# Optimization experiments

Hardware: AMD Instinct MI355X
Metric: run time of the kernel (lower is better)

Reference implementation:

```python
import jax, jax.numpy as jnp
import numpy as np

B, T, TA = 16, 512, 1024
D_REG, D_AUD, HID, HEADS = 512, 512, 256, 4
NREG = 4  # mouth, left_eye, right_eye, nose (dict order)
N = NREG * B * T + B * TA  # total graph nodes


def _build_edges():
    # Faithful, vectorized version of build_graph's edge construction (phoneme_times=None).
    bs = np.arange(B)[:, None]
    ts = np.arange(T)[None, :]
    src, dst = [], []
    # cross-region same-timestep edges, all ordered pairs i != j (edge_attr 0)
    for i in range(NREG):
        for j in range(NREG):
            if i != j:
                n1 = i * B * T + bs * T + ts
                n2 = j * B * T + bs * T + ts
                src.append(n1.ravel()); dst.append(n2.ravel())
    # temporal edges within each region (edge_attr 1)
    tt = np.arange(T - 1)[None, :]
    for i in range(NREG):
        n1 = i * B * T + bs * T + tt
        src.append(n1.ravel()); dst.append((n1 + 1).ravel())
    # eye (region idx 1,2) -> audio alignment edges (edge_attr 3)
    t_aud = (np.arange(T)[None, :] * TA) // T
    audio_start = NREG * B * T
    for i in (1, 2):
        n_eye = i * B * T + bs * T + ts
        n_aud = audio_start + bs * TA + t_aud
        src.append(n_eye.ravel()); dst.append(np.broadcast_to(n_aud, (B, T)).ravel())
    # self loops (PyG GATConv default add_self_loops=True)
    loops = np.arange(N)
    src.append(loops); dst.append(loops)
    return np.concatenate(src).astype(np.int32), np.concatenate(dst).astype(np.int32)


def setup_inputs() -> dict:
    key = jax.random.key(0)
    ks = iter(jax.random.split(key, 48))
    def rn(shape, scale=1.0):
        return jax.random.normal(next(ks), shape, dtype=jnp.float32) * jnp.float32(scale)
    src_np, dst_np = _build_edges()
    inp = {
        'mouth': rn((B, T, D_REG)), 'left_eye': rn((B, T, D_REG)),
        'right_eye': rn((B, T, D_REG)), 'nose': rn((B, T, D_REG)),
        'audio_embeddings': rn((B, TA, D_AUD)),
    }
    s = 1.0 / np.sqrt(D_REG)
    for name in ['mouth', 'left_eye', 'right_eye', 'nose']:
        inp['w_' + name] = rn((D_REG, HID), s)
        inp['b_' + name] = jnp.zeros((HID,), jnp.float32)
    inp['w_audio'] = rn((D_AUD, HID), 1.0 / np.sqrt(D_AUD))
    inp['b_audio'] = jnp.zeros((HID,), jnp.float32)
    # GAT layers: layer 0 in=HID, layers 1,2 in=HID*HEADS; layers 0,1 concat, layer 2 averages heads
    dims_in = [HID, HID * HEADS, HID * HEADS]
    for l, din in enumerate(dims_in):
        concat = l < 2
        inp[f'W{l}'] = rn((din, HEADS * HID), 1.0 / np.sqrt(din))
        inp[f'as{l}'] = rn((HEADS, HID), 0.1)
        inp[f'ad{l}'] = rn((HEADS, HID), 0.1)
        inp[f'bias{l}'] = jnp.zeros((HEADS * HID,) if concat else (HID,), jnp.float32)
    inp['ln_g'] = jnp.ones((HID,), jnp.float32)
    inp['ln_b'] = jnp.zeros((HID,), jnp.float32)
    inp['src'] = jnp.asarray(src_np)
    inp['dst'] = jnp.asarray(dst_np)
    return inp


def _gat(x, W, a_s, a_d, bias, src, dst, concat):
    # PyG GATConv (eval mode): gather -> per-head attention softmax over dst -> scatter-add
    H, C = a_s.shape
    h = (x @ W).reshape(-1, H, C)                      # [N,H,C]
    alpha_s = jnp.sum(h * a_s, -1)                     # [N,H]
    alpha_d = jnp.sum(h * a_d, -1)                     # [N,H]
    e = jax.nn.leaky_relu(alpha_s[src] + alpha_d[dst], 0.2)  # [E,H]
    m = jax.ops.segment_max(e, dst, num_segments=N)
    ex = jnp.exp(e - m[dst])
    denom = jax.ops.segment_sum(ex, dst, num_segments=N)
    alpha = ex / (denom[dst] + jnp.float32(1e-16))
    out = jax.ops.segment_sum(h[src] * alpha[:, :, None], dst, num_segments=N)  # [N,H,C]
    out = out.reshape(-1, H * C) if concat else out.mean(1)
    return out + bias


def _forward(mouth, left_eye, right_eye, nose, audio_embeddings,
             w_mouth, b_mouth, w_left_eye, b_left_eye, w_right_eye, b_right_eye,
             w_nose, b_nose, w_audio, b_audio,
             W0, as0, ad0, bias0, W1, as1, ad1, bias1, W2, as2, ad2, bias2,
             ln_g, ln_b, src, dst):
    x = jnp.concatenate([
        (mouth @ w_mouth + b_mouth).reshape(B * T, HID),
        (left_eye @ w_left_eye + b_left_eye).reshape(B * T, HID),
        (right_eye @ w_right_eye + b_right_eye).reshape(B * T, HID),
        (nose @ w_nose + b_nose).reshape(B * T, HID),
        (audio_embeddings @ w_audio + b_audio).reshape(B * TA, HID),
    ], axis=0)                                          # [N,HID]
    x = _gat(x, W0, as0, ad0, bias0, src, dst, True)    # [N,HID*HEADS]
    x = _gat(x, W1, as1, ad1, bias1, src, dst, True)    # [N,HID*HEADS]
    x = _gat(x, W2, as2, ad2, bias2, src, dst, False)   # [N,HID]
    mu = x.mean(-1, keepdims=True)
    var = jnp.mean(jnp.square(x - mu), -1, keepdims=True)
    x = (x - mu) / jnp.sqrt(var + jnp.float32(1e-5)) * ln_g + ln_b
    nodes_pb = NREG * T + TA
    return x.reshape(B, nodes_pb, HID).mean(1)          # [B,HID]


def reference(mouth, left_eye, right_eye, nose, audio_embeddings,
              w_mouth, b_mouth, w_left_eye, b_left_eye, w_right_eye, b_right_eye,
              w_nose, b_nose, w_audio, b_audio,
              W0, as0, ad0, bias0, W1, as1, ad1, bias1, W2, as2, ad2, bias2,
              ln_g, ln_b, src, dst):
    return _forward(mouth, left_eye, right_eye, nose, audio_embeddings,
                    w_mouth, b_mouth, w_left_eye, b_left_eye, w_right_eye, b_right_eye,
                    w_nose, b_nose, w_audio, b_audio,
                    W0, as0, ad0, bias0, W1, as1, ad1, bias1, W2, as2, ad2, bias2,
                    ln_g, ln_b, src, dst)
```

## Files before the change

### kernel.cpp

```cpp
#include <hip/hip_runtime.h>


typedef unsigned short u16;
typedef unsigned int u32;
typedef __bf16 bf16x8 __attribute__((ext_vector_type(8)));
typedef float f32x4 __attribute__((ext_vector_type(4)));

#define ASYNC16(gp, lp)                                                        \
  __builtin_amdgcn_global_load_lds(                                            \
      (const __attribute__((address_space(1))) void*)(gp),                     \
      (__attribute__((address_space(3))) void*)(lp), 16, 0, 0)

__device__ __forceinline__ u16 f2bf(float f) {
  union { float f; u32 u; } v; v.f = f;
  u32 u = v.u + 0x7FFFu + ((v.u >> 16) & 1u);
  return (u16)(u >> 16);
}
__device__ __forceinline__ float bf2f(u16 x) {
  union { u32 u; float f; } v; v.u = ((u32)x) << 16;
  return v.f;
}
__device__ __forceinline__ float4 cvt4(ushort4 s) {
  float4 r; r.x = bf2f(s.x); r.y = bf2f(s.y); r.z = bf2f(s.z); r.w = bf2f(s.w);
  return r;
}
__device__ __forceinline__ float lrelu(float v) { return v > 0.f ? v : 0.2f * v; }
__device__ __forceinline__ float dot4(float4 a, float4 b) {
  return a.x * b.x + a.y * b.y + a.z * b.z + a.w * b.w;
}
__device__ __forceinline__ float wred(float v) {
#pragma unroll
  for (int off = 32; off; off >>= 1) v += __shfl_down(v, off);
  return v;
}
__device__ __forceinline__ float wredx(float v) {
#pragma unroll
  for (int off = 32; off; off >>= 1) v += __shfl_xor(v, off);
  return v;
}

struct PK { const float* W[8]; u16* P[8]; int KB[8]; int NN[8]; int st[9]; };
__global__ __launch_bounds__(256) void pack_kernel(PK p) {
  const int f = blockIdx.x * 4 + (threadIdx.x >> 6);
  const int lane = threadIdx.x & 63;
  int e = 0;
  while (f >= p.st[e + 1]) ++e;
  const int local = f - p.st[e];
  const int KB = p.KB[e], N = p.NN[e];
  const int nt = local / KB, kb = local % KB;
  const float* W = p.W[e] + (size_t)(kb * 32 + (lane >> 4) * 8) * N + nt * 16 + (lane & 15);
  u16* dst = p.P[e] + ((size_t)local * 64 + lane) * 8;
  u16 o[8];
#pragma unroll
  for (int j = 0; j < 8; ++j) o[j] = f2bf(W[(size_t)j * N]);
  *(uint4*)dst = *(uint4*)o;
}

__global__ __launch_bounds__(256) void gemm_kernel(
    const u16* __restrict__ A, const u16* __restrict__ Bp, u16* __restrict__ C,
    int K, int ldc) {
  __shared__ __align__(16) u16 As[2][2][128 * 32];
  const int KB = K >> 5;
  const int KB2 = K >> 6;
  const int w = blockIdx.y * 8 + blockIdx.x;
  const int xcd = w & 7, m = w >> 3;
  const int blockCol = (m & 7) * 128;
  const int blockRow = ((m >> 3) * 8 + xcd) * 128;
  const int tid = threadIdx.x;
  const int wave = tid >> 6, lane = tid & 63;
  const int wr = (wave >> 1) * 64, wc = (wave & 1) * 64;
  const int lr = lane & 15, lq = lane >> 4;
  const int sRow = wave * 16 + (lane >> 2);
  const int sGc = (lane & 3) ^ ((sRow >> 1) & 3);
  const size_t aOff0 = (size_t)(blockRow + sRow) * K + sGc * 8;
  const size_t aOff1 = aOff0 + (size_t)64 * K;
  const int ldsOff0 = wave * 512;
  const int ldsOff1 = 2048 + wave * 512;

  const u16* Bn[4];
#pragma unroll
  for (int ni = 0; ni < 4; ++ni)
    Bn[ni] = Bp + ((size_t)(((blockCol + wc) >> 4) + ni) * KB) * 512 + lane * 8;

  f32x4 acc[4][4] = {};

#pragma unroll
  for (int h = 0; h < 2; ++h) {
    ASYNC16(A + aOff0 + h * 32, As[0][h] + ldsOff0);
    ASYNC16(A + aOff1 + h * 32, As[0][h] + ldsOff1);
  }
  __syncthreads();

  for (int kb2 = 0; kb2 < KB2; ++kb2) {
    const int cb = kb2 & 1;
    bf16x8 bfr[2][4];
#pragma unroll
    for (int h = 0; h < 2; ++h)
#pragma unroll
      for (int ni = 0; ni < 4; ++ni)
        bfr[h][ni] = *(const bf16x8*)(Bn[ni] + (size_t)(kb2 * 2 + h) * 512);
    if (kb2 + 1 < KB2) {
      const size_t k1 = (size_t)(kb2 + 1) * 64;
#pragma unroll
      for (int h = 0; h < 2; ++h) {
        ASYNC16(A + aOff0 + k1 + h * 32, As[cb ^ 1][h] + ldsOff0);
        ASYNC16(A + aOff1 + k1 + h * 32, As[cb ^ 1][h] + ldsOff1);
      }
    }
#pragma unroll
    for (int h = 0; h < 2; ++h) {
      const u16* cur = As[cb][h];
      bf16x8 af[4];
#pragma unroll
      for (int mi = 0; mi < 4; ++mi) {
        const int R = wr + mi * 16 + lr;
        const int cp = lq ^ ((R >> 1) & 3);
        af[mi] = *(const bf16x8*)(cur + R * 32 + cp * 8);
      }
#pragma unroll
      for (int mi = 0; mi < 4; ++mi)
#pragma unroll
        for (int ni = 0; ni < 4; ++ni)
          acc[mi][ni] = __builtin_amdgcn_mfma_f32_16x16x32_bf16(af[mi], bfr[h][ni],
                                                                acc[mi][ni], 0, 0, 0);
    }
    __syncthreads();
  }
#pragma unroll
  for (int mi = 0; mi < 4; ++mi)
#pragma unroll
    for (int ni = 0; ni < 4; ++ni) {
      const int col = blockCol + wc + ni * 16 + lr;
#pragma unroll
      for (int r = 0; r < 4; ++r) {
        const int row = blockRow + wr + mi * 16 + lq * 4 + r;
        C[(size_t)row * ldc + col] = f2bf(acc[mi][ni][r]);
      }
    }
}

struct ProjArgs { const float* x[5]; const u16* w[5]; const float* b[5]; };
__global__ __launch_bounds__(256) void proj_kernel(ProjArgs pa,
                                                   u16* __restrict__ C) {
  __shared__ __align__(16) u16 As[128 * 32];
  const int blockRow = blockIdx.y * 128, blockCol = blockIdx.x * 128;
  const int reg = blockRow >= 32768 ? 4 : (blockRow >> 13);
  const int regBase = reg == 4 ? 32768 : reg * 8192;
  const float* Af = pa.x[reg] + (size_t)(blockRow - regBase) * 512;
  const u16* Bp = pa.w[reg];
  const int tid = threadIdx.x;
  const int wave = tid >> 6, lane = tid & 63;
  const int wr = (wave >> 1) * 64, wc = (wave & 1) * 64;
  const int lr = lane & 15, lq = lane >> 4;
  const int rr = tid >> 2;
  const int cphys = tid & 3;
  const int sGc = cphys ^ ((tid >> 3) & 3);

  const u16* Bn[4];
#pragma unroll
  for (int ni = 0; ni < 4; ++ni)
    Bn[ni] = Bp + ((size_t)(((blockCol + wc) >> 4) + ni) * 16) * 512 + lane * 8;

  f32x4 acc[4][4] = {};

  for (int k0 = 0; k0 < 512; k0 += 32) {
    __syncthreads();
    bf16x8 bfr[4];
#pragma unroll
    for (int ni = 0; ni < 4; ++ni)
      bfr[ni] = *(const bf16x8*)(Bn[ni] + (size_t)k0 * 16);
#pragma unroll
    for (int i = 0; i < 2; ++i) {
      const int row = i * 64 + rr;
      const float* ap = Af + (size_t)row * 512 + k0 + sGc * 8;
      float4 f0 = *(const float4*)(ap);
      float4 f1 = *(const float4*)(ap + 4);
      uint4 pk;
      pk.x = (u32)f2bf(f0.x) | ((u32)f2bf(f0.y) << 16);
      pk.y = (u32)f2bf(f0.z) | ((u32)f2bf(f0.w) << 16);
      pk.z = (u32)f2bf(f1.x) | ((u32)f2bf(f1.y) << 16);
      pk.w = (u32)f2bf(f1.z) | ((u32)f2bf(f1.w) << 16);
      *(uint4*)(&As[row * 32 + cphys * 8]) = pk;
    }
    __syncthreads();
    bf16x8 af[4];
#pragma unroll
    for (int mi = 0; mi < 4; ++mi) {
      const int R = wr + mi * 16 + lr;
      const int cp = lq ^ ((R >> 1) & 3);
      af[mi] = *(const bf16x8*)(&As[R * 32 + cp * 8]);
    }
#pragma unroll
    for (int mi = 0; mi < 4; ++mi)
#pragma unroll
      for (int ni = 0; ni < 4; ++ni)
        acc[mi][ni] = __builtin_amdgcn_mfma_f32_16x16x32_bf16(af[mi], bfr[ni],
                                                              acc[mi][ni], 0, 0, 0);
  }
  const float* bias = pa.b[reg];
#pragma unroll
  for (int mi = 0; mi < 4; ++mi)
#pragma unroll
    for (int ni = 0; ni < 4; ++ni) {
      const int col = blockCol + wc + ni * 16 + lr;
      const float bv = bias[col];
#pragma unroll
      for (int r = 0; r < 4; ++r) {
        const int row = blockRow + wr + mi * 16 + lq * 4 + r;
        C[(size_t)row * 256 + col] = f2bf(acc[mi][ni][r] + bv);
      }
    }
}

template <bool MEAN>
__global__ __launch_bounds__(256) void agg_kernel(
    const u16* __restrict__ h, const float* __restrict__ a_s,
    const float* __restrict__ a_d, const float* __restrict__ bias,
    void* __restrict__ out) {
  extern __shared__ float red[];
  const int tid = threadIdx.x;
  const int head = tid >> 6, lane = tid & 63;
  const int c4 = tid * 4;
  const float4 sa = *(const float4*)(a_s + c4);
  const float4 da = *(const float4*)(a_d + c4);
  __shared__ float asL[4][4], adL[4][4], apL[4][4], aeS[4], aeD[4];
  __shared__ float alpha[4][4][5], alphaA[4][3];

  const int bt = blockIdx.x;
  const int b = bt >> 9, t = bt & 511;
  const bool hasPrev = t > 0;
  const int btp = hasPrev ? bt - 1 : bt;
  const int nodeE = 32768 + b * 1024 + 2 * t;
  const int nodeO = nodeE + 1;

  ushort4 rv[4], rp[4], raeR, raoR;
#pragma unroll
  for (int r = 0; r < 4; ++r)
    rv[r] = *(const ushort4*)(h + (size_t)(r * 8192 + bt) * 1024 + c4);
  raeR = *(const ushort4*)(h + (size_t)nodeE * 1024 + c4);
  raoR = *(const ushort4*)(h + (size_t)nodeO * 1024 + c4);
#pragma unroll
  for (int r = 0; r < 4; ++r)
    rp[r] = *(const ushort4*)(h + (size_t)(r * 8192 + btp) * 1024 + c4);

  float4 hv[4], hp[4];
#pragma unroll
  for (int r = 0; r < 4; ++r) hv[r] = cvt4(rv[r]);
  float4 hae = cvt4(raeR), hao = cvt4(raoR);
#pragma unroll
  for (int r = 0; r < 4; ++r) hp[r] = cvt4(rp[r]);

#pragma unroll
  for (int r = 0; r < 4; ++r) {
    float ss = wred(dot4(hv[r], sa));
    float dd = wred(dot4(hv[r], da));
    float sp = hasPrev ? wred(dot4(hp[r], sa)) : 0.f;
    if (lane == 0) { asL[r][head] = ss; adL[r][head] = dd; apL[r][head] = sp; }
  }
  {
    float se = wred(dot4(hae, sa));
    float de = wred(dot4(hae, da));
    if (lane == 0) { aeS[head] = se; aeD[head] = de; }
  }
  __syncthreads();
  if (tid < 16) {
    const int j = tid >> 2, hh = tid & 3;
    const float ad = adL[j][hh];
    float e[5];
#pragma unroll
    for (int r = 0; r < 4; ++r) e[r] = lrelu(asL[r][hh] + ad);
    int cnt = 4;
    if (hasPrev) { e[4] = lrelu(apL[j][hh] + ad); cnt = 5; }
    float mx = e[0];
    for (int k = 1; k < cnt; ++k) mx = fmaxf(mx, e[k]);
    float s = 0.f, ex[5];
    for (int k = 0; k < cnt; ++k) { ex[k] = __expf(e[k] - mx); s += ex[k]; }
    const float inv = 1.f / (s + 1e-16f);
#pragma unroll
    for (int k = 0; k < 5; ++k) alpha[j][hh][k] = (k < cnt) ? ex[k] * inv : 0.f;
  } else if (tid < 20) {
    const int hh = tid - 16;
    const float ad = aeD[hh];
    const float e0 = lrelu(aeS[hh] + ad);
    const float e1 = lrelu(asL[1][hh] + ad);
    const float e2 = lrelu(asL[2][hh] + ad);
    const float mx = fmaxf(e0, fmaxf(e1, e2));
    const float x0 = __expf(e0 - mx), x1 = __expf(e1 - mx), x2 = __expf(e2 - mx);
    const float inv = 1.f / (x0 + x1 + x2 + 1e-16f);
    alphaA[hh][0] = x0 * inv; alphaA[hh][1] = x1 * inv; alphaA[hh][2] = x2 * inv;
  }
  __syncthreads();

  float4 av[6];
#pragma unroll
  for (int j = 0; j < 4; ++j) {
    const float* al = &alpha[j][head][0];
    float4 acc;
    acc.x = al[0] * hv[0].x + al[1] * hv[1].x + al[2] * hv[2].x + al[3] * hv[3].x;
    acc.y = al[0] * hv[0].y + al[1] * hv[1].y + al[2] * hv[2].y + al[3] * hv[3].y;
    acc.z = al[0] * hv[0].z + al[1] * hv[1].z + al[2] * hv[2].z + al[3] * hv[3].z;
    acc.w = al[0] * hv[0].w + al[1] * hv[1].w + al[2] * hv[2].w + al[3] * hv[3].w;
    if (hasPrev) {
      const float a4 = al[4];
      acc.x += a4 * hp[j].x; acc.y += a4 * hp[j].y;
      acc.z += a4 * hp[j].z; acc.w += a4 * hp[j].w;
    }
    av[j] = acc;
  }
  {
    const float a0 = alphaA[head][0], a1 = alphaA[head][1], a2 = alphaA[head][2];
    float4 acc;
    acc.x = a0 * hae.x + a1 * hv[1].x + a2 * hv[2].x;
    acc.y = a0 * hae.y + a1 * hv[1].y + a2 * hv[2].y;
    acc.z = a0 * hae.z + a1 * hv[1].z + a2 * hv[2].z;
    acc.w = a0 * hae.w + a1 * hv[1].w + a2 * hv[2].w;
    av[4] = acc;
    av[5] = hao;
  }

  if constexpr (!MEAN) {
    const float4 bv = *(const float4*)(bias + c4);
    u16* ob = (u16*)out;
    size_t rows[6];
#pragma unroll
    for (int j = 0; j < 4; ++j) rows[j] = (size_t)(j * 8192 + bt);
    rows[4] = (size_t)nodeE; rows[5] = (size_t)nodeO;
#pragma unroll
    for (int k = 0; k < 6; ++k) {
      ushort4 o;
      o.x = f2bf(av[k].x + bv.x); o.y = f2bf(av[k].y + bv.y);
      o.z = f2bf(av[k].z + bv.z); o.w = f2bf(av[k].w + bv.w);
      *(ushort4*)(ob + rows[k] * 1024 + c4) = o;
    }
  } else {
#pragma unroll
    for (int k = 0; k < 6; ++k) *(float4*)(&red[k * 1024 + c4]) = av[k];
    __syncthreads();
    const float bb = bias[tid];
    float* of = (float*)out;
    size_t rows[6];
#pragma unroll
    for (int j = 0; j < 4; ++j) rows[j] = (size_t)(j * 8192 + bt);
    rows[4] = (size_t)nodeE; rows[5] = (size_t)nodeO;
#pragma unroll
    for (int k = 0; k < 6; ++k) {
      const float v = 0.25f * (red[k * 1024 + tid] + red[k * 1024 + tid + 256] +
                               red[k * 1024 + tid + 512] + red[k * 1024 + tid + 768]) + bb;
      of[rows[k] * 256 + tid] = v;
    }
  }
}

__global__ __launch_bounds__(256) void ln_pool_kernel(
    const float* __restrict__ xf, const float* __restrict__ g,
    const float* __restrict__ bb, float* __restrict__ part) {
  const int tid = threadIdx.x;
  const int wave = tid >> 6, lane = tid & 63;
  const int node0 = blockIdx.x * 64 + wave * 16;
  const float4 g4 = *(const float4*)(g + lane * 4);
  const float4 b4 = *(const float4*)(bb + lane * 4);
  float4 acc = {0.f, 0.f, 0.f, 0.f};
  for (int i = 0; i < 16; ++i) {
    const float4 v = *(const float4*)(xf + (size_t)(node0 + i) * 256 + lane * 4);
    const float s = wredx(v.x + v.y + v.z + v.w);
    const float q = wredx(v.x * v.x + v.y * v.y + v.z * v.z + v.w * v.w);
    const float mean = s * (1.f / 256.f);
    const float var = q * (1.f / 256.f) - mean * mean;
    const float rstd = rsqrtf(var + 1e-5f);
    acc.x += (v.x - mean) * rstd * g4.x + b4.x;
    acc.y += (v.y - mean) * rstd * g4.y + b4.y;
    acc.z += (v.z - mean) * rstd * g4.z + b4.z;
    acc.w += (v.w - mean) * rstd * g4.w + b4.w;
  }
  *(float4*)(part + (size_t)(blockIdx.x * 4 + wave) * 256 + lane * 4) = acc;
}

__global__ __launch_bounds__(256) void pool2_kernel(const float* __restrict__ part,
                                                    float* __restrict__ out) {
  const int chunk = blockIdx.x;
  const int c = threadIdx.x;
  float s = 0.f;
  for (int i = 0; i < 192; ++i) s += part[(size_t)(chunk * 192 + i) * 256 + c];
  out[chunk * 256 + c] = s * (1.f / 3072.f);
}

extern "C" void kernel_launch(void* const* d_in, const int* in_sizes, int n_in,
                              void* d_out, int out_size, void* d_ws, size_t ws_size,
                              hipStream_t stream) {
  const float* x_reg[4] = {(const float*)d_in[0], (const float*)d_in[1],
                           (const float*)d_in[2], (const float*)d_in[3]};
  const float* audio = (const float*)d_in[4];
  const float* w_reg[4] = {(const float*)d_in[5], (const float*)d_in[7],
                           (const float*)d_in[9], (const float*)d_in[11]};
  const float* b_reg[4] = {(const float*)d_in[6], (const float*)d_in[8],
                           (const float*)d_in[10], (const float*)d_in[12]};
  const float* w_aud = (const float*)d_in[13];
  const float* b_aud = (const float*)d_in[14];
  const float* Wl[3] = {(const float*)d_in[15], (const float*)d_in[19],
                        (const float*)d_in[23]};
  const float* as_in[3] = {(const float*)d_in[16], (const float*)d_in[20],
                           (const float*)d_in[24]};
  const float* ad_in[3] = {(const float*)d_in[17], (const float*)d_in[21],
                           (const float*)d_in[25]};
  const float* bias_l[3] = {(const float*)d_in[18], (const float*)d_in[22],
                            (const float*)d_in[26]};
  const float* ln_g = (const float*)d_in[27];
  const float* ln_b = (const float*)d_in[28];

  char* ws = (char*)d_ws;
  u16* h_bf = (u16*)ws;
  float* part = (float*)ws;
  u16* xb = (u16*)(ws + 100663296);
  float* xf = (float*)xb;
  u16* wt = (u16*)(ws + 201326592);

  u16* wtp[5];
  for (int r = 0; r < 5; ++r) wtp[r] = wt + (size_t)r * 131072;
  u16* wt0 = wt + 655360;
  u16* wt1 = wt + 917504;
  u16* wt2 = wt + 1966080;

  PK pk;
  for (int r = 0; r < 4; ++r) { pk.W[r] = w_reg[r]; pk.P[r] = wtp[r]; pk.KB[r] = 16; pk.NN[r] = 256; }
  pk.W[4] = w_aud; pk.P[4] = wtp[4]; pk.KB[4] = 16; pk.NN[4] = 256;
  pk.W[5] = Wl[0]; pk.P[5] = wt0; pk.KB[5] = 8;  pk.NN[5] = 1024;
  pk.W[6] = Wl[1]; pk.P[6] = wt1; pk.KB[6] = 32; pk.NN[6] = 1024;
  pk.W[7] = Wl[2]; pk.P[7] = wt2; pk.KB[7] = 32; pk.NN[7] = 1024;
  pk.st[0] = 0;
  {
    const int nfr[8] = {256, 256, 256, 256, 256, 512, 2048, 2048};
    int acc = 0;
    for (int e = 0; e < 8; ++e) { acc += nfr[e]; pk.st[e + 1] = acc; }
  }
  pack_kernel<<<pk.st[8] / 4, 256, 0, stream>>>(pk);

  ProjArgs pa;
  for (int r = 0; r < 4; ++r) { pa.x[r] = x_reg[r]; pa.w[r] = wtp[r]; pa.b[r] = b_reg[r]; }
  pa.x[4] = audio; pa.w[4] = wtp[4]; pa.b[4] = b_aud;
  proj_kernel<<<dim3(2, 384), 256, 0, stream>>>(pa, xb);

  const u16* wl[3] = {wt0, wt1, wt2};
  const int Kl[3] = {256, 1024, 1024};
  const size_t dynLds = 6 * 1024 * sizeof(float);
  for (int l = 0; l < 3; ++l) {
    gemm_kernel<<<dim3(8, 384), 256, 0, stream>>>(xb, wl[l], h_bf, Kl[l], 1024);
    if (l < 2)
      agg_kernel<false><<<8192, 256, 0, stream>>>(h_bf, as_in[l], ad_in[l],
                                                  bias_l[l], xb);
    else
      agg_kernel<true><<<8192, 256, dynLds, stream>>>(h_bf, as_in[l], ad_in[l],
                                                      bias_l[l], xf);
  }

  ln_pool_kernel<<<768, 256, 0, stream>>>(xf, ln_g, ln_b, part);
  pool2_kernel<<<16, 256, 0, stream>>>(part, (float*)d_out);
}
```

Measured before the change: 613.5 us.

## Templatize GEMM on K with occupancy hints, remap agg block order, reduce pool partials in-block

```diff
diff --git a/kernel.cpp b/kernel.cpp
--- a/kernel.cpp
+++ b/kernel.cpp
@@ -56,12 +56,13 @@
   *(uint4*)dst = *(uint4*)o;
 }
 
-__global__ __launch_bounds__(256) void gemm_kernel(
-    const u16* __restrict__ A, const u16* __restrict__ Bp, u16* __restrict__ C,
-    int K, int ldc) {
+template <int K, int MINW>
+__global__ __launch_bounds__(256, MINW) void gemm_kernel(
+    const u16* __restrict__ A, const u16* __restrict__ Bp, u16* __restrict__ C) {
+  constexpr int ldc = 1024;
+  constexpr int KB = K >> 5;
+  constexpr int KB2 = K >> 6;
   __shared__ __align__(16) u16 As[2][2][128 * 32];
-  const int KB = K >> 5;
-  const int KB2 = K >> 6;
   const int w = blockIdx.y * 8 + blockIdx.x;
   const int xcd = w & 7, m = w >> 3;
   const int blockCol = (m & 7) * 128;
@@ -226,7 +227,8 @@
   __shared__ float asL[4][4], adL[4][4], apL[4][4], aeS[4], aeD[4];
   __shared__ float alpha[4][4][5], alphaA[4][3];
 
-  const int bt = blockIdx.x;
+  const int bid = blockIdx.x;
+  const int bt = ((bid & 7) << 10) | (bid >> 3);
   const int b = bt >> 9, t = bt & 511;
   const bool hasPrev = t > 0;
   const int btp = hasPrev ? bt - 1 : bt;
@@ -354,6 +356,7 @@
 __global__ __launch_bounds__(256) void ln_pool_kernel(
     const float* __restrict__ xf, const float* __restrict__ g,
     const float* __restrict__ bb, float* __restrict__ part) {
+  __shared__ float sh[1024];
   const int tid = threadIdx.x;
   const int wave = tid >> 6, lane = tid & 63;
   const int node0 = blockIdx.x * 64 + wave * 16;
@@ -372,7 +375,10 @@
     acc.z += (v.z - mean) * rstd * g4.z + b4.z;
     acc.w += (v.w - mean) * rstd * g4.w + b4.w;
   }
-  *(float4*)(part + (size_t)(blockIdx.x * 4 + wave) * 256 + lane * 4) = acc;
+  *(float4*)(&sh[wave * 256 + lane * 4]) = acc;
+  __syncthreads();
+  const float s = sh[tid] + sh[256 + tid] + sh[512 + tid] + sh[768 + tid];
+  part[(size_t)blockIdx.x * 256 + tid] = s;
 }
 
 __global__ __launch_bounds__(256) void pool2_kernel(const float* __restrict__ part,
@@ -380,7 +386,7 @@
   const int chunk = blockIdx.x;
   const int c = threadIdx.x;
   float s = 0.f;
-  for (int i = 0; i < 192; ++i) s += part[(size_t)(chunk * 192 + i) * 256 + c];
+  for (int i = 0; i < 48; ++i) s += part[(size_t)(chunk * 48 + i) * 256 + c];
   out[chunk * 256 + c] = s * (1.f / 3072.f);
 }
 
@@ -439,18 +445,13 @@
   pa.x[4] = audio; pa.w[4] = wtp[4]; pa.b[4] = b_aud;
   proj_kernel<<<dim3(2, 384), 256, 0, stream>>>(pa, xb);
 
-  const u16* wl[3] = {wt0, wt1, wt2};
-  const int Kl[3] = {256, 1024, 1024};
   const size_t dynLds = 6 * 1024 * sizeof(float);
-  for (int l = 0; l < 3; ++l) {
-    gemm_kernel<<<dim3(8, 384), 256, 0, stream>>>(xb, wl[l], h_bf, Kl[l], 1024);
-    if (l < 2)
-      agg_kernel<false><<<8192, 256, 0, stream>>>(h_bf, as_in[l], ad_in[l],
-                                                  bias_l[l], xb);
-    else
-      agg_kernel<true><<<8192, 256, dynLds, stream>>>(h_bf, as_in[l], ad_in[l],
-                                                      bias_l[l], xf);
-  }
+  gemm_kernel<256, 4><<<dim3(8, 384), 256, 0, stream>>>(xb, wt0, h_bf);
+  agg_kernel<false><<<8192, 256, 0, stream>>>(h_bf, as_in[0], ad_in[0], bias_l[0], xb);
+  gemm_kernel<1024, 4><<<dim3(8, 384), 256, 0, stream>>>(xb, wt1, h_bf);
+  agg_kernel<false><<<8192, 256, 0, stream>>>(h_bf, as_in[1], ad_in[1], bias_l[1], xb);
+  gemm_kernel<1024, 1><<<dim3(8, 384), 256, 0, stream>>>(xb, wt2, h_bf);
+  agg_kernel<true><<<8192, 256, dynLds, stream>>>(h_bf, as_in[2], ad_in[2], bias_l[2], xf);
 
   ln_pool_kernel<<<768, 256, 0, stream>>>(xf, ln_g, ln_b, part);
   pool2_kernel<<<16, 256, 0, stream>>>(part, (float*)d_out);
```

New measurement: 605.9 us. Within noise of the previous version (-1.2%).
